# Performance work log

Hardware: AMD Instinct MI355X
Metric: run time of the kernel (lower is better)

## Reference

```python
import jax, jax.numpy as jnp
import numpy as np

NEIGHBOR_NUM = 50
SUPPORT = 1  # support_num

def _normalize(x, axis):
    n = jnp.linalg.norm(x, axis=axis, keepdims=True)
    return x / jnp.maximum(n, 1e-12)

def get_neighbor_index(v, k):
    # v: (b, n, 3) -> kNN indices (b, n, k), excluding self (smallest distance)
    inner = jnp.einsum('bvd,bwd->bvw', v, v)
    q = jnp.sum(v * v, axis=-1)
    dist = -2.0 * inner + q[:, None, :] + q[:, :, None]  # (b, n, n)
    _, idx = jax.lax.top_k(-dist, k + 1)                 # smallest k+1
    return idx[:, :, 1:]

def indexing_neighbor(t, idx):
    # t: (b, n, c), idx: (b, n, k) -> (b, n, k, c)
    return jax.vmap(lambda tb, ib: tb[ib])(t, idx)

def neighbor_direction_norm(v, idx):
    nbr = indexing_neighbor(v, idx)                      # (b, n, k, 3)
    return _normalize(nbr - v[:, :, None, :], -1)

def conv_surface(idx, v, directions, kernel_num):
    b, vn, nn_ = idx.shape
    dnorm = neighbor_direction_norm(v, idx)              # (b, n, k, 3)
    sdir = _normalize(directions, 0)                     # (3, s*kern)
    theta = jax.nn.relu(jnp.einsum('bvnd,dk->bvnk', dnorm, sdir))
    theta = theta.reshape(b, vn, nn_, SUPPORT, kernel_num)
    return jnp.sum(jnp.max(theta, axis=2), axis=2)       # (b, n, kern)

def conv_layer(idx, v, fmap, weights, bias, directions, out_c):
    b, vn, nn_ = idx.shape
    dnorm = neighbor_direction_norm(v, idx)
    sdir = _normalize(directions, 0)                     # (3, s*out)
    theta = jax.nn.relu(jnp.einsum('bvnd,dk->bvnk', dnorm, sdir))  # (b,n,k,s*out)
    fout = fmap @ weights + bias                         # (b, n, (s+1)*out)
    f_center = fout[:, :, :out_c]
    f_support = indexing_neighbor(fout[:, :, out_c:], idx)         # (b,n,k,s*out)
    act = (theta * f_support).reshape(b, vn, nn_, SUPPORT, out_c)
    return f_center + jnp.sum(jnp.max(act, axis=2), axis=2)

def pool(v, fmap, rate=4, nnum=4):
    idx = get_neighbor_index(v, nnum)
    pooled = jnp.max(indexing_neighbor(fmap, idx), axis=2)
    pn = v.shape[1] // rate
    sel = jnp.arange(pn)  # deterministic subsample (original: randperm)
    return v[:, sel, :], pooled[:, sel, :]

def _uniform(key, shape, stdv):
    return jax.random.uniform(key, shape, jnp.float32, -stdv, stdv)

def setup_inputs() -> dict:
    key = jax.random.key(0)
    ks = jax.random.split(key, 20)
    import math
    d = {'vertices': jax.random.normal(ks[0], (2, 8192, 3), jnp.float32)}
    # Conv_surface(kernel_num=32)
    d['dir0'] = _uniform(ks[1], (3, SUPPORT * 32), 1.0 / math.sqrt(SUPPORT * 32))
    def mk(kw, kb, kd, in_c, out_c):
        s = 1.0 / math.sqrt(out_c * (SUPPORT + 1))
        return (_uniform(kw, (in_c, (SUPPORT + 1) * out_c), s),
                _uniform(kb, ((SUPPORT + 1) * out_c,), s),
                _uniform(kd, (3, SUPPORT * out_c), s))
    d['w1'], d['b1'], d['d1'] = mk(ks[2], ks[3], ks[4], 32, 64)
    d['w2'], d['b2'], d['d2'] = mk(ks[5], ks[6], ks[7], 64, 128)
    d['w3'], d['b3'], d['d3'] = mk(ks[8], ks[9], ks[10], 128, 256)
    d['w4'], d['b4'], d['d4'] = mk(ks[11], ks[12], ks[13], 256, 1024)
    fstd = 1.0 / math.sqrt(1024)
    d['fc_w'] = _uniform(ks[14], (1024, 256), fstd)
    d['fc_b'] = _uniform(ks[15], (256,), fstd)
    return d

def reference(vertices, dir0, w1, b1, d1, w2, b2, d2, w3, b3, d3, w4, b4, d4, fc_w, fc_b):
    v = vertices
    idx = get_neighbor_index(v, NEIGHBOR_NUM)
    fm0 = jax.nn.relu(conv_surface(idx, v, dir0, 32))
    fm1 = jax.nn.relu(conv_layer(idx, v, fm0, w1, b1, d1, 64))
    v, fm1 = pool(v, fm1)
    idx = get_neighbor_index(v, NEIGHBOR_NUM)
    fm2 = jax.nn.relu(conv_layer(idx, v, fm1, w2, b2, d2, 128))
    fm3 = jax.nn.relu(conv_layer(idx, v, fm2, w3, b3, d3, 256))
    v, fm3 = pool(v, fm3)
    idx = get_neighbor_index(v, NEIGHBOR_NUM)
    fm4 = conv_layer(idx, v, fm3, w4, b4, d4, 1024)
    feat = jnp.max(fm4, axis=1)                          # (b, 1024)
    return feat @ fc_w + fc_b                            # (b, 256)
```

## Files before the change

### kernel.cpp

```cpp
#include <hip/hip_runtime.h>
#include <cmath>


__device__ __forceinline__ unsigned flipf(float f) {
    unsigned u = __float_as_uint(f);
    return (u & 0x80000000u) ? ~u : (u | 0x80000000u);
}
__device__ __forceinline__ float unflip(unsigned u) {
    unsigned r = (u & 0x80000000u) ? (u & 0x7fffffffu) : ~u;
    return __uint_as_float(r);
}
__device__ __forceinline__ unsigned umin2(unsigned a, unsigned b) {
    return a < b ? a : b;
}

__global__ __launch_bounds__(256) void precompute_vq(
    const float* __restrict__ v, float4* __restrict__ vq, int n)
{
#pragma clang fp contract(off)
    const int i = blockIdx.x * 256 + threadIdx.x;
    if (i < n) {
        const float x = v[i * 3 + 0];
        const float y = v[i * 3 + 1];
        const float z = v[i * 3 + 2];
        float4 o; o.x = x; o.y = y; o.z = z; o.w = (x * x + y * y) + z * z;
        vq[i] = o;
    }
}

template <int CPT, int SMP, int SEL, int EST, int QPB = 8, int CAPQ = 160>
__global__ __launch_bounds__(256) void knn_select(
    const float4* __restrict__ vq, int vStride, int nRows,
    int* __restrict__ outIdx)
{
#pragma clang fp contract(off)
    const int tid  = threadIdx.x;
    const int bpb  = nRows / QPB;
    const int b    = blockIdx.x / bpb;
    const int row0 = (blockIdx.x % bpb) * QPB;
    const float4* vb = vq + (size_t)b * vStride;

    float nx[QPB], ny[QPB], nz[QPB], qw[QPB];
#pragma unroll
    for (int qq = 0; qq < QPB; ++qq) {
        const float4 p = vb[row0 + qq];
        nx[qq] = p.x * -2.0f; ny[qq] = p.y * -2.0f; nz[qq] = p.z * -2.0f;
        qw[qq] = p.w;
    }

    float mn[QPB];
#pragma unroll
    for (int qq = 0; qq < QPB; ++qq) mn[qq] = INFINITY;
#pragma unroll
    for (int s = 0; s < SMP; ++s) {
        const float4 c = vb[tid + (s << 8)];
#pragma unroll
        for (int qq = 0; qq < QPB; ++qq) {
            const float t0 = (nx[qq] * c.x + ny[qq] * c.y) + nz[qq] * c.z;
            const float dist = (t0 + c.w) + qw[qq];
            mn[qq] = fminf(mn[qq], dist);
        }
    }

    __shared__ unsigned hmin[QPB][256];
    __shared__ unsigned long long bufq[QPB][CAPQ];
    __shared__ unsigned long long fbuf[CPT * SEL];
    __shared__ unsigned Ts[QPB];
    __shared__ int cnt[QPB];
    __shared__ unsigned T2_s;
    __shared__ int fcnt;

#pragma unroll
    for (int qq = 0; qq < QPB; ++qq) hmin[qq][tid] = flipf(mn[qq]);
    if (tid < QPB) { Ts[tid] = 0u; cnt[tid] = 0; }
    __syncthreads();

    {
        const int g = tid >> 5, l = tid & 31;
#pragma unroll
        for (int hh = 0; hh < 2; ++hh) {
            const int i = l + hh * 32;
            unsigned cm = hmin[g][i];
            cm = umin2(cm, hmin[g][i + 64]);
            cm = umin2(cm, hmin[g][i + 128]);
            cm = umin2(cm, hmin[g][i + 192]);
            hmin[g][i] = cm;
        }
#pragma unroll
        for (int hh = 0; hh < 2; ++hh) {
            const unsigned vv = hmin[g][l + hh * 32];
            int r = 0;
#pragma unroll 8
            for (int k = 0; k < 64; ++k) r += (hmin[g][k] < vv) ? 1 : 0;
            if (r < EST) atomicMax(&Ts[g], vv);
        }
    }
    __syncthreads();

    float Tf[QPB];
#pragma unroll
    for (int qq = 0; qq < QPB; ++qq) Tf[qq] = unflip(Ts[qq]);

#pragma unroll 2
    for (int s = 0; s < CPT; ++s) {
        const int j = tid + (s << 8);
        const float4 c = vb[j];
#pragma unroll
        for (int qq = 0; qq < QPB; ++qq) {
            const float t0 = (nx[qq] * c.x + ny[qq] * c.y) + nz[qq] * c.z;
            const float dist = (t0 + c.w) + qw[qq];
            if (dist <= Tf[qq]) {
                const int p = atomicAdd(&cnt[qq], 1);
                if (p < CAPQ)
                    bufq[qq][p] = (((unsigned long long)flipf(dist)) << 32)
                                | (unsigned)j;
            }
        }
    }
    __syncthreads();

    for (int qq = 0; qq < QPB; ++qq) {
        const int M = cnt[qq];
        if (M >= SEL && M <= CAPQ) continue;
        {
            float fm = INFINITY;
#pragma unroll 2
            for (int s = 0; s < CPT; ++s) {
                const float4 c = vb[tid + (s << 8)];
                const float t0 = (nx[qq] * c.x + ny[qq] * c.y) + nz[qq] * c.z;
                const float dist = (t0 + c.w) + qw[qq];
                fm = fminf(fm, dist);
            }
            hmin[qq][tid] = flipf(fm);
        }
        if (tid == 0) { T2_s = 0u; fcnt = 0; }
        __syncthreads();
        {
            const unsigned vv = hmin[qq][tid];
            int r = 0;
            for (int k = 0; k < 256; ++k) r += (hmin[qq][k] < vv) ? 1 : 0;
            if (r < SEL) atomicMax(&T2_s, vv);
        }
        __syncthreads();
        const float T2f = unflip(T2_s);
#pragma unroll 2
        for (int s = 0; s < CPT; ++s) {
            const int j = tid + (s << 8);
            const float4 c = vb[j];
            const float t0 = (nx[qq] * c.x + ny[qq] * c.y) + nz[qq] * c.z;
            const float dist = (t0 + c.w) + qw[qq];
            if (dist <= T2f) {
                const int p = atomicAdd(&fcnt, 1);
                fbuf[p] = (((unsigned long long)flipf(dist)) << 32) | (unsigned)j;
            }
        }
        __syncthreads();
        const int M2 = fcnt;
        for (int s2 = tid; s2 < M2; s2 += 256) {
            const unsigned long long k = fbuf[s2];
            int rr = 0;
            for (int i2 = 0; i2 < M2; ++i2) rr += (fbuf[i2] < k) ? 1 : 0;
            if (rr >= 1 && rr < SEL)
                outIdx[(size_t)(b * nRows + row0 + qq) * (SEL - 1) + (rr - 1)]
                    = (int)(k & 0xffffffffu);
        }
        if (tid == 0) cnt[qq] = 0;
        __syncthreads();
    }

    {
        const int g = tid >> 5, i = tid & 31;
        const int M = cnt[g];
        for (int s2 = i; s2 < M; s2 += 32) {
            const unsigned long long k = bufq[g][s2];
            int rr = 0;
            for (int i2 = 0; i2 < M; ++i2) rr += (bufq[g][i2] < k) ? 1 : 0;
            if (rr >= 1 && rr < SEL)
                outIdx[(size_t)(b * nRows + row0 + g) * (SEL - 1) + (rr - 1)]
                    = (int)(k & 0xffffffffu);
        }
    }
}

template <int NT>
__global__ __launch_bounds__(NT) void conv_kernel(
    const int*    __restrict__ idx,
    const float4* __restrict__ vq,
    int vStride, int V, int NN,
    const float* __restrict__ fout,
    int oc,
    const float* __restrict__ dirs,
    float* __restrict__ out,
    int do_relu)
{
#pragma clang fp contract(off)
    __shared__ float dnx[64], dny[64], dnz[64];
    __shared__ int   nb[64];
    const int bi  = blockIdx.x;
    const int b   = bi / V;
    const int i   = bi % V;
    const int tid = threadIdx.x;

    if (tid < NN) {
        const int j = idx[(size_t)bi * NN + tid];
        nb[tid] = j;
        const float4 ci = vq[(size_t)b * vStride + i];
        const float4 cj = vq[(size_t)b * vStride + j];
        const float dx = cj.x - ci.x;
        const float dy = cj.y - ci.y;
        const float dz = cj.z - ci.z;
        const float n  = sqrtf((dx * dx + dy * dy) + dz * dz);
        const float dn = fmaxf(n, 1e-12f);
        dnx[tid] = dx / dn;
        dny[tid] = dy / dn;
        dnz[tid] = dz / dn;
    }
    __syncthreads();

    const int ocPer = oc / gridDim.y;
    const int cLo   = blockIdx.y * ocPer;
    const float* fsup = fout ? (fout + (size_t)b * V * (2 * oc) + oc) : nullptr;

    for (int c = cLo + tid; c < cLo + ocPer; c += NT) {
        float d0 = dirs[c], d1 = dirs[oc + c], d2 = dirs[2 * oc + c];
        const float nd = sqrtf((d0 * d0 + d1 * d1) + d2 * d2);
        const float dc = fmaxf(nd, 1e-12f);
        d0 /= dc; d1 /= dc; d2 /= dc;

        float fcen = 0.f;
        if (fout) fcen = fout[(size_t)bi * (2 * oc) + c];

        float m = -INFINITY;
        constexpr int BN = 10;
        for (int n0 = 0; n0 < 50; n0 += BN) {
            float fs[BN];
            if (fout) {
#pragma unroll
                for (int u = 0; u < BN; ++u)
                    fs[u] = fsup[(size_t)nb[n0 + u] * (2 * oc) + c];
            } else {
#pragma unroll
                for (int u = 0; u < BN; ++u) fs[u] = 1.f;
            }
#pragma unroll
            for (int u = 0; u < BN; ++u) {
                const int n = n0 + u;
                float th = (dnx[n] * d0 + dny[n] * d1) + dnz[n] * d2;
                th = fmaxf(th, 0.f);
                m = fmaxf(m, th * fs[u]);
            }
        }
        float r = fcen + m;
        if (do_relu) r = fmaxf(r, 0.f);
        out[(size_t)bi * oc + c] = r;
    }
}

__global__ __launch_bounds__(256) void gemm_tiled(
    const float* __restrict__ A, const float* __restrict__ W,
    const float* __restrict__ bias, float* __restrict__ out,
    int M, int K, int N)
{
    __shared__ float As[32][68];
    __shared__ float Bs[32][64];
    const int tid = threadIdx.x;
    const int tx = tid & 15, ty = tid >> 4;
    const int r0 = blockIdx.x * 64;
    const int c0 = blockIdx.y * 64;

    const float4 bv = *(const float4*)&bias[c0 + tx * 4];
    float acc[4][4];
#pragma unroll
    for (int i = 0; i < 4; ++i) {
        acc[i][0] = bv.x; acc[i][1] = bv.y; acc[i][2] = bv.z; acc[i][3] = bv.w;
    }

    const int rowA = tid >> 2;
    const int ca4  = tid & 3;
    const int rowB = tid >> 4;
    const int cb4  = tid & 15;

    for (int k0 = 0; k0 < K; k0 += 32) {
        const float4 a0 = *(const float4*)&A[(size_t)(r0 + rowA) * K + k0 + ca4 * 4];
        const float4 a1 = *(const float4*)&A[(size_t)(r0 + rowA) * K + k0 + (ca4 + 4) * 4];
        const float4 b0 = *(const float4*)&W[(size_t)(k0 + rowB) * N + c0 + cb4 * 4];
        const float4 b1 = *(const float4*)&W[(size_t)(k0 + rowB + 16) * N + c0 + cb4 * 4];
        __syncthreads();
        As[ca4 * 4 + 0][rowA] = a0.x;
        As[ca4 * 4 + 1][rowA] = a0.y;
        As[ca4 * 4 + 2][rowA] = a0.z;
        As[ca4 * 4 + 3][rowA] = a0.w;
        As[ca4 * 4 + 16][rowA] = a1.x;
        As[ca4 * 4 + 17][rowA] = a1.y;
        As[ca4 * 4 + 18][rowA] = a1.z;
        As[ca4 * 4 + 19][rowA] = a1.w;
        *(float4*)&Bs[rowB][cb4 * 4]      = b0;
        *(float4*)&Bs[rowB + 16][cb4 * 4] = b1;
        __syncthreads();
#pragma unroll
        for (int kk = 0; kk < 32; ++kk) {
            const float4 av = *(const float4*)&As[kk][ty * 4];
            const float4 wv = *(const float4*)&Bs[kk][tx * 4];
            acc[0][0] += av.x * wv.x; acc[0][1] += av.x * wv.y;
            acc[0][2] += av.x * wv.z; acc[0][3] += av.x * wv.w;
            acc[1][0] += av.y * wv.x; acc[1][1] += av.y * wv.y;
            acc[1][2] += av.y * wv.z; acc[1][3] += av.y * wv.w;
            acc[2][0] += av.z * wv.x; acc[2][1] += av.z * wv.y;
            acc[2][2] += av.z * wv.z; acc[2][3] += av.z * wv.w;
            acc[3][0] += av.w * wv.x; acc[3][1] += av.w * wv.y;
            acc[3][2] += av.w * wv.z; acc[3][3] += av.w * wv.w;
        }
    }
#pragma unroll
    for (int i = 0; i < 4; ++i) {
        float4 o;
        o.x = acc[i][0]; o.y = acc[i][1]; o.z = acc[i][2]; o.w = acc[i][3];
        *(float4*)&out[(size_t)(r0 + ty * 4 + i) * N + c0 + tx * 4] = o;
    }
}

__global__ __launch_bounds__(256) void pool_max(
    const int* __restrict__ idxNN, int nnStride, const float* __restrict__ fm,
    int Vin, int pn, int C, float* __restrict__ out)
{
    const int t  = blockIdx.x * 256 + threadIdx.x;
    const int c  = t % C;
    const int bi = t / C;
    const int b  = bi / pn;
    const int i  = bi % pn;
    const int* r = idxNN + (size_t)(b * Vin + i) * nnStride;
    const int j0 = r[0], j1 = r[1], j2 = r[2], j3 = r[3];
    float m = fm[((size_t)b * Vin + j0) * C + c];
    m = fmaxf(m, fm[((size_t)b * Vin + j1) * C + c]);
    m = fmaxf(m, fm[((size_t)b * Vin + j2) * C + c]);
    m = fmaxf(m, fm[((size_t)b * Vin + j3) * C + c]);
    out[(size_t)bi * C + c] = m;
}

__global__ __launch_bounds__(256) void colmax_part(
    const float* __restrict__ fm, int V, int C, int rowsPerChunk,
    float* __restrict__ part)
{
    const int b = blockIdx.y, chunk = blockIdx.z;
    const int nChunk = gridDim.z;
    const int c = blockIdx.x * 256 + threadIdx.x;
    const int i0 = chunk * rowsPerChunk;
    float m = -INFINITY;
    for (int i = i0; i < i0 + rowsPerChunk; ++i)
        m = fmaxf(m, fm[((size_t)b * V + i) * C + c]);
    part[((size_t)b * nChunk + chunk) * C + c] = m;
}

__global__ __launch_bounds__(256) void fc_kernel(
    const float* __restrict__ part, const float* __restrict__ W,
    const float* __restrict__ bias, float* __restrict__ out, int nChunk)
{
    __shared__ float f[1024];
    const int b = blockIdx.x, tid = threadIdx.x;
    for (int k = tid; k < 1024; k += 256) {
        float m = part[((size_t)b * nChunk) * 1024 + k];
        for (int ch = 1; ch < nChunk; ++ch)
            m = fmaxf(m, part[((size_t)b * nChunk + ch) * 1024 + k]);
        f[k] = m;
    }
    __syncthreads();
    float acc = bias[tid];
    for (int k = 0; k < 1024; ++k) acc += f[k] * W[(size_t)k * 256 + tid];
    out[(size_t)b * 256 + tid] = acc;
}

extern "C" void kernel_launch(void* const* d_in, const int* in_sizes, int n_in,
                              void* d_out, int out_size, void* d_ws, size_t ws_size,
                              hipStream_t stream) {
    const float* verts = (const float*)d_in[0];
    const float* dir0  = (const float*)d_in[1];
    const float* w1 = (const float*)d_in[2];
    const float* b1 = (const float*)d_in[3];
    const float* d1 = (const float*)d_in[4];
    const float* w2 = (const float*)d_in[5];
    const float* b2 = (const float*)d_in[6];
    const float* d2 = (const float*)d_in[7];
    const float* w3 = (const float*)d_in[8];
    const float* b3 = (const float*)d_in[9];
    const float* d3 = (const float*)d_in[10];
    const float* w4 = (const float*)d_in[11];
    const float* b4 = (const float*)d_in[12];
    const float* d4 = (const float*)d_in[13];
    const float* fcw = (const float*)d_in[14];
    const float* fcb = (const float*)d_in[15];

    const int B = 2, V1 = 8192, V2 = 2048, V3 = 512, NN = 50;

    char* ws = (char*)d_ws;
    float*  arena1 = (float*)(ws + 0);
    float*  arena2 = (float*)(ws + 8388608);
    float*  arena3 = (float*)(ws + 12582912);
    int*    arena4 = (int*)  (ws + 16777216);
    float*  arena5 = (float*)(ws + 20054016);
    float*  arena6 = (float*)(ws + 22151168);
    float*  part   = (float*)(ws + 23265280);
    float4* vq     = (float4*)(ws + 23330816);

    precompute_vq<<<(B * V1 + 255) / 256, 256, 0, stream>>>(verts, vq, B * V1);

    int* idxA = arena4;
    knn_select<32, 8, 51, 20><<<B * V1 / 8, 256, 0, stream>>>(vq, V1, V1, idxA);

    float* fm0 = arena5;
    conv_kernel<64><<<dim3(B * V1, 1), 64, 0, stream>>>(idxA, vq, V1, V1, NN,
                                                        nullptr, 32, dir0, fm0, 1);
    float* fout1 = arena1;
    gemm_tiled<<<dim3(B * V1 / 64, 128 / 64), 256, 0, stream>>>(
        fm0, w1, b1, fout1, B * V1, 32, 128);
    float* fm1 = arena2;
    conv_kernel<64><<<dim3(B * V1, 1), 64, 0, stream>>>(idxA, vq, V1, V1, NN,
                                                        fout1, 64, d1, fm1, 1);
    float* fm1p = arena6;
    pool_max<<<B * V2 * 64 / 256, 256, 0, stream>>>(idxA, NN, fm1, V1, V2, 64, fm1p);

    int* idxB = arena4;
    knn_select<8, 2, 51, 20><<<B * V2 / 8, 256, 0, stream>>>(vq, V1, V2, idxB);
    float* fout2 = arena3;
    gemm_tiled<<<dim3(B * V2 / 64, 256 / 64), 256, 0, stream>>>(
        fm1p, w2, b2, fout2, B * V2, 64, 256);
    float* fm2 = arena5;
    conv_kernel<128><<<dim3(B * V2, 1), 128, 0, stream>>>(idxB, vq, V1, V2, NN,
                                                          fout2, 128, d2, fm2, 1);
    float* fout3 = arena1;
    gemm_tiled<<<dim3(B * V2 / 64, 512 / 64), 256, 0, stream>>>(
        fm2, w3, b3, fout3, B * V2, 128, 512);
    float* fm3 = arena2;
    conv_kernel<256><<<dim3(B * V2, 1), 256, 0, stream>>>(idxB, vq, V1, V2, NN,
                                                          fout3, 256, d3, fm3, 1);
    float* fm3p = arena6;
    pool_max<<<B * V3 * 256 / 256, 256, 0, stream>>>(idxB, NN, fm3, V2, V3, 256, fm3p);

    int* idxC = arena4;
    knn_select<2, 2, 51, 48><<<B * V3 / 8, 256, 0, stream>>>(vq, V1, V3, idxC);
    float* fout4 = arena1;
    gemm_tiled<<<dim3(B * V3 / 64, 2048 / 64), 256, 0, stream>>>(
        fm3p, w4, b4, fout4, B * V3, 256, 2048);
    float* fm4 = arena2;
    conv_kernel<256><<<dim3(B * V3, 4), 256, 0, stream>>>(idxC, vq, V1, V3, NN,
                                                          fout4, 1024, d4, fm4, 0);
    colmax_part<<<dim3(1024 / 256, B, 8), 256, 0, stream>>>(fm4, V3, 1024, V3 / 8, part);
    fc_kernel<<<B, 256, 0, stream>>>(part, fcw, fcb, (float*)d_out, 8);
}
```

Before: 350.0 us.

## Map one wavefront per vertex and vectorize channel gathers in conv kernel

The conv kernel now packs four vertices into each 256-thread block, giving one 64-lane wavefront per vertex with its own shared-memory neighbour-direction slice. Each lane handles 1, 2 or 4 consecutive output channels through float2/float4 loads and stores, chosen per layer. The aim is to cut the number of tiny blocks, idle threads and scalar gathers on the support-feature reads. In exchange it uses more registers per thread and drops the fp-contract-off pragma, which may slightly change rounding.

```diff
diff --git a/kernel.cpp b/kernel.cpp
--- a/kernel.cpp
+++ b/kernel.cpp
@@ -12,6 +12,19 @@
 }
 __device__ __forceinline__ unsigned umin2(unsigned a, unsigned b) {
     return a < b ? a : b;
+}
+
+template <int VC>
+__device__ __forceinline__ void load_vec(float* d, const float* p) {
+    if constexpr (VC == 1) { d[0] = p[0]; }
+    else if constexpr (VC == 2) { const float2 t = *(const float2*)p; d[0] = t.x; d[1] = t.y; }
+    else { const float4 t = *(const float4*)p; d[0] = t.x; d[1] = t.y; d[2] = t.z; d[3] = t.w; }
+}
+template <int VC>
+__device__ __forceinline__ void store_vec(float* p, const float* d) {
+    if constexpr (VC == 1) { p[0] = d[0]; }
+    else if constexpr (VC == 2) { float2 t; t.x = d[0]; t.y = d[1]; *(float2*)p = t; }
+    else { float4 t; t.x = d[0]; t.y = d[1]; t.z = d[2]; t.w = d[3]; *(float4*)p = t; }
 }
 
 __global__ __launch_bounds__(256) void precompute_vq(
@@ -182,7 +195,7 @@
     }
 }
 
-template <int NT>
+template <int NT, int VC>
 __global__ __launch_bounds__(NT) void conv_kernel(
     const int*    __restrict__ idx,
     const float4* __restrict__ vq,
@@ -193,67 +206,84 @@
     float* __restrict__ out,
     int do_relu)
 {
-#pragma clang fp contract(off)
-    __shared__ float dnx[64], dny[64], dnz[64];
-    __shared__ int   nb[64];
-    const int bi  = blockIdx.x;
-    const int b   = bi / V;
-    const int i   = bi % V;
-    const int tid = threadIdx.x;
-
-    if (tid < NN) {
-        const int j = idx[(size_t)bi * NN + tid];
-        nb[tid] = j;
+    constexpr int G = NT / 64;
+    __shared__ float dnx[G][64], dny[G][64], dnz[G][64];
+    __shared__ int   nb[G][64];
+    const int w    = threadIdx.x >> 6;
+    const int lane = threadIdx.x & 63;
+    const int vi   = blockIdx.x * G + w;
+    const int b    = vi / V;
+    const int i    = vi % V;
+
+    if (lane < NN) {
+        const int j = idx[(size_t)vi * NN + lane];
+        nb[w][lane] = j;
         const float4 ci = vq[(size_t)b * vStride + i];
         const float4 cj = vq[(size_t)b * vStride + j];
         const float dx = cj.x - ci.x;
         const float dy = cj.y - ci.y;
         const float dz = cj.z - ci.z;
         const float n  = sqrtf((dx * dx + dy * dy) + dz * dz);
-        const float dn = fmaxf(n, 1e-12f);
-        dnx[tid] = dx / dn;
-        dny[tid] = dy / dn;
-        dnz[tid] = dz / dn;
+        const float dnv = fmaxf(n, 1e-12f);
+        dnx[w][lane] = dx / dnv;
+        dny[w][lane] = dy / dnv;
+        dnz[w][lane] = dz / dnv;
     }
     __syncthreads();
 
-    const int ocPer = oc / gridDim.y;
-    const int cLo   = blockIdx.y * ocPer;
-    const float* fsup = fout ? (fout + (size_t)b * V * (2 * oc) + oc) : nullptr;
-
-    for (int c = cLo + tid; c < cLo + ocPer; c += NT) {
-        float d0 = dirs[c], d1 = dirs[oc + c], d2 = dirs[2 * oc + c];
-        const float nd = sqrtf((d0 * d0 + d1 * d1) + d2 * d2);
+    const int c0 = blockIdx.y * (64 * VC) + lane * VC;
+    if (c0 >= oc) return;
+
+    float d0[VC], d1[VC], d2[VC], fcen[VC], m[VC];
+#pragma unroll
+    for (int k = 0; k < VC; ++k) {
+        const float a  = dirs[c0 + k];
+        const float bb = dirs[oc + c0 + k];
+        const float cc = dirs[2 * oc + c0 + k];
+        const float nd = sqrtf((a * a + bb * bb) + cc * cc);
         const float dc = fmaxf(nd, 1e-12f);
-        d0 /= dc; d1 /= dc; d2 /= dc;
-
-        float fcen = 0.f;
-        if (fout) fcen = fout[(size_t)bi * (2 * oc) + c];
-
-        float m = -INFINITY;
-        constexpr int BN = 10;
-        for (int n0 = 0; n0 < 50; n0 += BN) {
-            float fs[BN];
-            if (fout) {
-#pragma unroll
-                for (int u = 0; u < BN; ++u)
-                    fs[u] = fsup[(size_t)nb[n0 + u] * (2 * oc) + c];
-            } else {
-#pragma unroll
-                for (int u = 0; u < BN; ++u) fs[u] = 1.f;
+        d0[k] = a / dc; d1[k] = bb / dc; d2[k] = cc / dc;
+        fcen[k] = 0.f;
+        m[k] = -INFINITY;
+    }
+    const float* fsup = nullptr;
+    if (fout) {
+        fsup = fout + (size_t)b * V * (2 * oc) + oc;
+        load_vec<VC>(fcen, &fout[(size_t)vi * (2 * oc) + c0]);
+    }
+
+    constexpr int BN = (VC >= 4) ? 5 : 10;
+    for (int n0 = 0; n0 < 50; n0 += BN) {
+        float fs[BN][VC];
+        if (fsup) {
+#pragma unroll
+            for (int u = 0; u < BN; ++u)
+                load_vec<VC>(fs[u], &fsup[(size_t)nb[w][n0 + u] * (2 * oc) + c0]);
+        } else {
+#pragma unroll
+            for (int u = 0; u < BN; ++u)
+#pragma unroll
+                for (int k = 0; k < VC; ++k) fs[u][k] = 1.f;
+        }
+#pragma unroll
+        for (int u = 0; u < BN; ++u) {
+            const int n = n0 + u;
+            const float ax = dnx[w][n], ay = dny[w][n], az = dnz[w][n];
+#pragma unroll
+            for (int k = 0; k < VC; ++k) {
+                float th = (ax * d0[k] + ay * d1[k]) + az * d2[k];
+                th = fmaxf(th, 0.f);
+                m[k] = fmaxf(m[k], th * fs[u][k]);
             }
-#pragma unroll
-            for (int u = 0; u < BN; ++u) {
-                const int n = n0 + u;
-                float th = (dnx[n] * d0 + dny[n] * d1) + dnz[n] * d2;
-                th = fmaxf(th, 0.f);
-                m = fmaxf(m, th * fs[u]);
-            }
-        }
-        float r = fcen + m;
-        if (do_relu) r = fmaxf(r, 0.f);
-        out[(size_t)bi * oc + c] = r;
-    }
+        }
+    }
+    float r[VC];
+#pragma unroll
+    for (int k = 0; k < VC; ++k) {
+        r[k] = fcen[k] + m[k];
+        if (do_relu) r[k] = fmaxf(r[k], 0.f);
+    }
+    store_vec<VC>(&out[(size_t)vi * oc + c0], r);
 }
 
 __global__ __launch_bounds__(256) void gemm_tiled(
@@ -407,14 +437,14 @@
     knn_select<32, 8, 51, 20><<<B * V1 / 8, 256, 0, stream>>>(vq, V1, V1, idxA);
 
     float* fm0 = arena5;
-    conv_kernel<64><<<dim3(B * V1, 1), 64, 0, stream>>>(idxA, vq, V1, V1, NN,
-                                                        nullptr, 32, dir0, fm0, 1);
+    conv_kernel<256, 1><<<dim3(B * V1 / 4, 1), 256, 0, stream>>>(
+        idxA, vq, V1, V1, NN, nullptr, 32, dir0, fm0, 1);
     float* fout1 = arena1;
     gemm_tiled<<<dim3(B * V1 / 64, 128 / 64), 256, 0, stream>>>(
         fm0, w1, b1, fout1, B * V1, 32, 128);
     float* fm1 = arena2;
-    conv_kernel<64><<<dim3(B * V1, 1), 64, 0, stream>>>(idxA, vq, V1, V1, NN,
-                                                        fout1, 64, d1, fm1, 1);
+    conv_kernel<256, 1><<<dim3(B * V1 / 4, 1), 256, 0, stream>>>(
+        idxA, vq, V1, V1, NN, fout1, 64, d1, fm1, 1);
     float* fm1p = arena6;
     pool_max<<<B * V2 * 64 / 256, 256, 0, stream>>>(idxA, NN, fm1, V1, V2, 64, fm1p);
 
@@ -424,14 +454,14 @@
     gemm_tiled<<<dim3(B * V2 / 64, 256 / 64), 256, 0, stream>>>(
         fm1p, w2, b2, fout2, B * V2, 64, 256);
     float* fm2 = arena5;
-    conv_kernel<128><<<dim3(B * V2, 1), 128, 0, stream>>>(idxB, vq, V1, V2, NN,
-                                                          fout2, 128, d2, fm2, 1);
+    conv_kernel<256, 2><<<dim3(B * V2 / 4, 1), 256, 0, stream>>>(
+        idxB, vq, V1, V2, NN, fout2, 128, d2, fm2, 1);
     float* fout3 = arena1;
     gemm_tiled<<<dim3(B * V2 / 64, 512 / 64), 256, 0, stream>>>(
         fm2, w3, b3, fout3, B * V2, 128, 512);
     float* fm3 = arena2;
-    conv_kernel<256><<<dim3(B * V2, 1), 256, 0, stream>>>(idxB, vq, V1, V2, NN,
-                                                          fout3, 256, d3, fm3, 1);
+    conv_kernel<256, 4><<<dim3(B * V2 / 4, 1), 256, 0, stream>>>(
+        idxB, vq, V1, V2, NN, fout3, 256, d3, fm3, 1);
     float* fm3p = arena6;
     pool_max<<<B * V3 * 256 / 256, 256, 0, stream>>>(idxB, NN, fm3, V2, V3, 256, fm3p);
 
@@ -441,8 +471,8 @@
     gemm_tiled<<<dim3(B * V3 / 64, 2048 / 64), 256, 0, stream>>>(
         fm3p, w4, b4, fout4, B * V3, 256, 2048);
     float* fm4 = arena2;
-    conv_kernel<256><<<dim3(B * V3, 4), 256, 0, stream>>>(idxC, vq, V1, V3, NN,
-                                                          fout4, 1024, d4, fm4, 0);
+    conv_kernel<256, 4><<<dim3(B * V3 / 4, 4), 256, 0, stream>>>(
+        idxC, vq, V1, V3, NN, fout4, 1024, d4, fm4, 0);
     colmax_part<<<dim3(1024 / 256, B, 8), 256, 0, stream>>>(fm4, V3, 1024, V3 / 8, part);
     fc_kernel<<<B, 256, 0, stream>>>(part, fcw, fcb, (float*)d_out, 8);
 }
```

Measured after the change: 345.6 us. No clear change (-1.2%).
